# Optimization experiments

Hardware: AMD Instinct MI355X
Metric: run time of the kernel (lower is better)

## Reference

```python
import jax, jax.numpy as jnp
import numpy as np

EPS = 1e-8

def setup_inputs() -> dict:
    key = jax.random.key(0)
    k1, k2, k3 = jax.random.split(key, 3)
    B, N, M = 4, 8192, 8192
    source = jax.random.normal(k1, (B, N, 3), dtype=jnp.float32)
    target = jax.random.normal(k2, (B, M, 3), dtype=jnp.float32)
    weights = jax.random.uniform(k3, (B, N), dtype=jnp.float32)
    return {"source": source, "target": target, "weights": weights}

def reference(source, target, weights):
    # Pairwise squared distances: (B, N, M)
    diff = source[:, :, None, :] - target[:, None, :, :]
    sq_distances = jnp.sum(diff * diff, axis=-1)
    # squared=False -> take sqrt with eps for stability
    distances = jnp.sqrt(sq_distances + EPS)
    # source -> target nearest-neighbor distance, weighted
    s2t = jnp.min(distances, axis=2) * weights  # (B, N)
    forward_loss = jnp.mean(s2t)
    # symmetric=True: target -> source (unweighted, as in original)
    t2s = jnp.min(distances, axis=1)  # (B, M)
    backward_loss = jnp.mean(t2s)
    return forward_loss + backward_loss
```

## Files before the change

kernel.cpp:

```cpp
#include <hip/hip_runtime.h>
#include <math.h>


#define EPS 1e-8f

typedef _Float16 f16x8 __attribute__((ext_vector_type(8)));
typedef float    f32x16 __attribute__((ext_vector_type(16)));

constexpr int B_    = 4;
constexpr int N_    = 8192;
constexpr int TPB   = 256;
constexpr int QPW   = 128;
constexpr int QPB   = 4 * QPW;
constexpr int RCH   = 16;
constexpr int CHUNK = N_ / RCH;
constexpr int RB    = 64;

__global__ __launch_bounds__(TPB, 6)
void nn_mfma_kernel(const float* __restrict__ src, const float* __restrict__ tgt,
                    unsigned int* __restrict__ minA, unsigned int* __restrict__ minB)
{
    __shared__ f16x8 sref[CHUNK + 64];

    const int zb  = blockIdx.z;
    const int dir = zb >> 2;
    const int b   = zb & 3;
    const float* Rraw = (dir ? src : tgt) + ((size_t)b * N_ + (size_t)blockIdx.y * CHUNK) * 3;
    const float* Qraw = (dir ? tgt : src) + (size_t)b * N_ * 3;
    unsigned int* omin = (dir ? minB : minA) + (size_t)b * N_;

    const int tid = threadIdx.x;
    const _Float16 h0 = (_Float16)0.f;
    const _Float16 h1 = (_Float16)1.f;

    for (int k = tid; k < CHUNK; k += TPB) {
        const float* rp = Rraw + (size_t)k * 3;
        _Float16 hx = (_Float16)rp[0], hy = (_Float16)rp[1], hz = (_Float16)rp[2];
        float fx = (float)hx, fy = (float)hy, fz = (float)hz;
        float rsq = fx * fx + fy * fy + fz * fz;
        _Float16 rh = (_Float16)rsq;
        _Float16 rl = (_Float16)(rsq - (float)rh);
        f16x8 a = {(_Float16)(-2.f * fx), (_Float16)(-2.f * fy),
                   (_Float16)(-2.f * fz), rh, rl, h0, h0, h0};
        sref[k] = a;
    }
    if (tid < 64) {
        f16x8 z = {h0, h0, h0, h0, h0, h0, h0, h0};
        sref[CHUNK + tid] = z;
    }

    const int lane = tid & 63;
    const int wv   = tid >> 6;
    const int l31  = lane & 31;
    const int half = lane >> 5;
    const int qb   = blockIdx.x * QPB + wv * QPW;

    f16x8 Bq[4];
    float qs[4];
#pragma unroll
    for (int t = 0; t < 4; ++t) {
        Bq[t] = f16x8{h0, h0, h0, h0, h0, h0, h0, h0};
        qs[t] = 0.f;
    }
    if (half == 0) {
#pragma unroll
        for (int t = 0; t < 4; ++t) {
            const float* q = Qraw + (size_t)(qb + t * 32 + l31) * 3;
            _Float16 ax = (_Float16)q[0], ay = (_Float16)q[1], az = (_Float16)q[2];
            float fx = (float)ax, fy = (float)ay, fz = (float)az;
            Bq[t] = f16x8{ax, ay, az, h1, h1, h0, h0, h0};
            qs[t] = fx * fx + fy * fy + fz * fz;
        }
    }
    __syncthreads();

    const f32x16 zc = {};

    int idx = (half == 0) ? l31 : CHUNK;
    const int step = (half == 0) ? 32 : 0;
    float mna[4] = {3.0e38f, 3.0e38f, 3.0e38f, 3.0e38f};
    float mnb[4] = {3.0e38f, 3.0e38f, 3.0e38f, 3.0e38f};

    f16x8 a = sref[idx];
    idx += step;
    for (int s = 0; s < CHUNK / 32; ++s) {
        f16x8 an = sref[idx];
        idx += step;
        f32x16 d0 = __builtin_amdgcn_mfma_f32_32x32x16_f16(a, Bq[0], zc, 0, 0, 0);
        f32x16 d1 = __builtin_amdgcn_mfma_f32_32x32x16_f16(a, Bq[1], zc, 0, 0, 0);
#pragma unroll
        for (int r = 0; r < 8; r += 2)
            mna[0] = fminf(fminf(d0[r], d0[r + 1]), mna[0]);
#pragma unroll
        for (int r = 8; r < 16; r += 2)
            mnb[0] = fminf(fminf(d0[r], d0[r + 1]), mnb[0]);
        f32x16 d2 = __builtin_amdgcn_mfma_f32_32x32x16_f16(a, Bq[2], zc, 0, 0, 0);
#pragma unroll
        for (int r = 0; r < 8; r += 2)
            mna[1] = fminf(fminf(d1[r], d1[r + 1]), mna[1]);
#pragma unroll
        for (int r = 8; r < 16; r += 2)
            mnb[1] = fminf(fminf(d1[r], d1[r + 1]), mnb[1]);
        f32x16 d3 = __builtin_amdgcn_mfma_f32_32x32x16_f16(a, Bq[3], zc, 0, 0, 0);
#pragma unroll
        for (int r = 0; r < 8; r += 2)
            mna[2] = fminf(fminf(d2[r], d2[r + 1]), mna[2]);
#pragma unroll
        for (int r = 8; r < 16; r += 2)
            mnb[2] = fminf(fminf(d2[r], d2[r + 1]), mnb[2]);
#pragma unroll
        for (int r = 0; r < 8; r += 2)
            mna[3] = fminf(fminf(d3[r], d3[r + 1]), mna[3]);
#pragma unroll
        for (int r = 8; r < 16; r += 2)
            mnb[3] = fminf(fminf(d3[r], d3[r + 1]), mnb[3]);
        a = an;
    }

#pragma unroll
    for (int t = 0; t < 4; ++t) {
        float mn = fminf(mna[t], mnb[t]);
        mn = fminf(mn, __shfl_xor(mn, 32));
        if (half == 0)
            atomicMin(&omin[qb + t * 32 + l31],
                      __float_as_uint(fmaxf(mn + qs[t], 0.f)));
    }
}

__global__ __launch_bounds__(TPB)
void reduce_kernel(const unsigned int* __restrict__ minA,
                   const unsigned int* __restrict__ minB,
                   const float* __restrict__ w,
                   float* __restrict__ out)
{
    const int BN = B_ * N_;
    const float invBN = 1.0f / (float)BN;

    float sum = 0.0f;
    for (int t = blockIdx.x * TPB + threadIdx.x; t < BN; t += RB * TPB) {
        sum += sqrtf(__uint_as_float(minA[t]) + EPS) * w[t];
        sum += sqrtf(__uint_as_float(minB[t]) + EPS);
    }
    sum *= invBN;

    __shared__ float ss[TPB / 64];
    int lane = threadIdx.x & 63;
    int wid  = threadIdx.x >> 6;
#pragma unroll
    for (int off = 32; off > 0; off >>= 1) sum += __shfl_down(sum, off);
    if (lane == 0) ss[wid] = sum;
    __syncthreads();
    if (threadIdx.x == 0) {
        float s = 0.0f;
#pragma unroll
        for (int i = 0; i < TPB / 64; ++i) s += ss[i];
        atomicAdd(out, s);
    }
}

extern "C" void kernel_launch(void* const* d_in, const int* in_sizes, int n_in,
                              void* d_out, int out_size, void* d_ws, size_t ws_size,
                              hipStream_t stream)
{
    const float* src = (const float*)d_in[0];
    const float* tgt = (const float*)d_in[1];
    const float* w   = (const float*)d_in[2];
    float* out = (float*)d_out;

    const size_t BN = (size_t)B_ * N_;
    unsigned int* minA = (unsigned int*)d_ws;
    unsigned int* minB = minA + BN;

    hipMemsetAsync(minA, 0x7F, 2 * BN * sizeof(unsigned int), stream);
    hipMemsetAsync(out, 0, sizeof(float), stream);

    dim3 grid(N_ / QPB, RCH, 2 * B_);
    nn_mfma_kernel<<<grid, TPB, 0, stream>>>(src, tgt, minA, minB);

    reduce_kernel<<<RB, TPB, 0, stream>>>(minA, minB, w, out);
}
```

Before: 77.09 us.

## Replace atomicMin and memsets with per-chunk partial minima reduced in final kernel

Each block now writes its per-query partial minimum to its own slot in a workspace array instead of doing atomicMin into a pre-memset buffer, and the reduce kernel takes the min across reference chunks. This removes two memset launches and the atomic traffic. The reference split is halved (larger chunks, fewer blocks) and the occupancy hint is lowered to fit the bigger shared buffer. The output zeroing moves into the main kernel. The reduce kernel now reads more data.

```diff
diff --git a/kernel.cpp b/kernel.cpp
--- a/kernel.cpp
+++ b/kernel.cpp
@@ -12,22 +12,25 @@
 constexpr int TPB   = 256;
 constexpr int QPW   = 128;
 constexpr int QPB   = 4 * QPW;
-constexpr int RCH   = 16;
+constexpr int RCH   = 8;
 constexpr int CHUNK = N_ / RCH;
 constexpr int RB    = 64;
 
-__global__ __launch_bounds__(TPB, 6)
+__global__ __launch_bounds__(TPB, 4)
 void nn_mfma_kernel(const float* __restrict__ src, const float* __restrict__ tgt,
-                    unsigned int* __restrict__ minA, unsigned int* __restrict__ minB)
+                    float* __restrict__ part, float* __restrict__ out)
 {
     __shared__ f16x8 sref[CHUNK + 64];
+
+    if (blockIdx.x == 0 && blockIdx.y == 0 && blockIdx.z == 0 && threadIdx.x == 0)
+        out[0] = 0.f;
 
     const int zb  = blockIdx.z;
     const int dir = zb >> 2;
     const int b   = zb & 3;
     const float* Rraw = (dir ? src : tgt) + ((size_t)b * N_ + (size_t)blockIdx.y * CHUNK) * 3;
     const float* Qraw = (dir ? tgt : src) + (size_t)b * N_ * 3;
-    unsigned int* omin = (dir ? minB : minA) + (size_t)b * N_;
+    float* opart = part + ((size_t)zb * RCH + blockIdx.y) * N_;
 
     const int tid = threadIdx.x;
     const _Float16 h0 = (_Float16)0.f;
@@ -122,24 +125,28 @@
         float mn = fminf(mna[t], mnb[t]);
         mn = fminf(mn, __shfl_xor(mn, 32));
         if (half == 0)
-            atomicMin(&omin[qb + t * 32 + l31],
-                      __float_as_uint(fmaxf(mn + qs[t], 0.f)));
+            opart[qb + t * 32 + l31] = fmaxf(mn + qs[t], 0.f);
     }
 }
 
 __global__ __launch_bounds__(TPB)
-void reduce_kernel(const unsigned int* __restrict__ minA,
-                   const unsigned int* __restrict__ minB,
+void reduce_kernel(const float* __restrict__ part,
                    const float* __restrict__ w,
                    float* __restrict__ out)
 {
-    const int BN = B_ * N_;
-    const float invBN = 1.0f / (float)BN;
+    const int Q = 2 * B_ * N_;
+    const float invBN = 1.0f / (float)(B_ * N_);
 
     float sum = 0.0f;
-    for (int t = blockIdx.x * TPB + threadIdx.x; t < BN; t += RB * TPB) {
-        sum += sqrtf(__uint_as_float(minA[t]) + EPS) * w[t];
-        sum += sqrtf(__uint_as_float(minB[t]) + EPS);
+    for (int t = blockIdx.x * TPB + threadIdx.x; t < Q; t += RB * TPB) {
+        const int zb = t >> 13;
+        const int qn = t & (N_ - 1);
+        const float* p = part + ((size_t)zb * RCH) * N_ + qn;
+        float m = p[0];
+#pragma unroll
+        for (int c = 1; c < RCH; ++c) m = fminf(m, p[(size_t)c * N_]);
+        float d = sqrtf(m + EPS);
+        sum += (zb < 4) ? d * w[(size_t)zb * N_ + qn] : d;
     }
     sum *= invBN;
 
@@ -167,15 +174,10 @@
     const float* w   = (const float*)d_in[2];
     float* out = (float*)d_out;
 
-    const size_t BN = (size_t)B_ * N_;
-    unsigned int* minA = (unsigned int*)d_ws;
-    unsigned int* minB = minA + BN;
-
-    hipMemsetAsync(minA, 0x7F, 2 * BN * sizeof(unsigned int), stream);
-    hipMemsetAsync(out, 0, sizeof(float), stream);
+    float* part = (float*)d_ws;
 
     dim3 grid(N_ / QPB, RCH, 2 * B_);
-    nn_mfma_kernel<<<grid, TPB, 0, stream>>>(src, tgt, minA, minB);
+    nn_mfma_kernel<<<grid, TPB, 0, stream>>>(src, tgt, part, out);
 
-    reduce_kernel<<<RB, TPB, 0, stream>>>(minA, minB, w, out);
+    reduce_kernel<<<RB, TPB, 0, stream>>>(part, w, out);
 }
```

New measurement: 76.32 us. No clear change (-1.0%).
